# Performance work log

Measured on AMD Instinct MI355X. Metric: run time of the kernel, lower is better.

## Reference

```python
import jax, jax.numpy as jnp
import numpy as np

S, M, E, K, C = 4096, 512, 16, 2, 128
H1, H2, H3 = 500, 500, 2000
SAMPLE = int(np.percentile(np.arange(S), 90))  # = 3685, matches int(np.percentile(idx_set, 90))
KMUL, KNUM = 2.0, 5


def setup_inputs() -> dict:
    key = jax.random.key(0)
    ks = jax.random.split(key, 8)
    def init(k, shape, fan):
        return (jax.random.normal(k, shape, jnp.float32) / np.float32(np.sqrt(fan)))
    inp = {
        'x': jax.random.normal(ks[0], (S, M), jnp.float32),
        'noise': jax.random.uniform(ks[1], (S, E), jnp.float32),
        'Wr': jnp.zeros((E, M), jnp.float32),  # router weight is zeroed in reset_parameters
        'W1': init(ks[2], (E, H1, M), M), 'b1': jnp.zeros((E, H1), jnp.float32),
        'W2': init(ks[3], (E, H2, H1), H1), 'b2': jnp.zeros((E, H2), jnp.float32),
        'W3': init(ks[4], (E, H3, H2), H2), 'b3': jnp.zeros((E, H3), jnp.float32),
        'W4': init(ks[5], (E, C, H3), H3), 'b4': jnp.zeros((E, C), jnp.float32),
    }
    rng = np.random.RandomState(0)
    npairs = K * (K - 1) // 2
    inp['idx1'] = jnp.asarray(np.stack([rng.choice(S, SAMPLE, replace=False) for _ in range(npairs)]).astype(np.int32))
    inp['idx2'] = jnp.asarray(np.stack([rng.choice(S, SAMPLE, replace=False) for _ in range(npairs)]).astype(np.int32))
    return inp


def _mmd(source, target):
    # Gaussian-kernel MMD, same math as MMD_loss (fix_sigma=None path).
    ns = source.shape[0]
    n = ns + target.shape[0]
    total = jnp.concatenate([source, target], axis=0)            # [n, d]
    sq = jnp.sum(total * total, axis=-1)
    d2 = sq[:, None] + sq[None, :] - 2.0 * (total @ total.T)     # [n, n] squared L2
    bw = jax.lax.stop_gradient(d2).sum() / (n * n - n)           # .data in torch => stop_gradient
    bw = bw / (KMUL ** (KNUM // 2))
    kern = jnp.zeros_like(d2)
    for i in range(KNUM):
        kern = kern + jnp.exp(-d2 / (bw * (KMUL ** i)))
    xx = kern[:ns, :ns]
    yy = kern[ns:, ns:]
    xy = kern[:ns, ns:]
    yx = kern[ns:, :ns]
    return jnp.mean(xx + yy - xy - yx)


def _forward(x, noise, Wr, W1, b1, W2, b2, W3, b3, W4, b4, idx1, idx2):
    select = x @ Wr.T + noise                                    # [S, E]
    gate, index = jax.lax.top_k(select, K)                       # [S, K]
    mask = jax.nn.one_hot(index, E, dtype=select.dtype)          # [S, K, E]
    density = mask.mean(axis=-2)                                 # [S, E]
    density_proxy = select.mean(axis=-2)                         # [E]
    balance_loss = jnp.mean(density_proxy * density) * float(E ** 2)
    mask_flat = mask.sum(axis=-1)                                # [S, K] (all ones)
    combine = jnp.transpose(gate[..., None] * mask_flat[..., None] * mask, (0, 2, 1))  # [S, E, K]
    dispatch = (combine != 0).astype(combine.dtype)              # bool().to(dtype)
    select0 = dispatch
    expert_inputs = jnp.einsum('sm,sec->ecm', x, dispatch)       # [E, K, M]
    h = jax.nn.relu(jnp.einsum('ecm,ehm->ech', expert_inputs, W1) + b1[:, None, :])
    h = jax.nn.relu(jnp.einsum('ech,egh->ecg', h, W2) + b2[:, None, :])
    h = jax.nn.relu(jnp.einsum('ecg,efg->ecf', h, W3) + b3[:, None, :])
    eout = jnp.einsum('ecf,edf->ecd', h, W4) + b4[:, None, :]    # [E, K, C]
    middle = jnp.transpose(jnp.einsum('sec,ecm->scm', combine, eout), (1, 0, 2))  # [K, S, C]
    output = jnp.einsum('sec,ecm->sm', combine, eout)            # [S, C]
    dist_loss = jnp.float32(0.0)
    p = 0
    for i in range(K):
        for j in range(i + 1, K):
            dist_loss = dist_loss - _mmd(middle[i][idx1[p]], middle[j][idx2[p]])
            p += 1
    return output, select0, balance_loss, dist_loss


def reference(x, noise, Wr, W1, b1, W2, b2, W3, b3, W4, b4, idx1, idx2):
    return _forward(x, noise, Wr, W1, b1, W2, b2, W3, b3, W4, b4, idx1, idx2)
```

## Files before the change

kernel.cpp:

```cpp
#include <hip/hip_runtime.h>

constexpr int S = 4096, M = 512, E = 16, CC = 128;
constexpr int H1 = 500, H2 = 500, H3 = 2000;

__global__ void k_route(const float* __restrict__ x, const float* __restrict__ noise,
                        const float* __restrict__ Wr, int* __restrict__ i0, int* __restrict__ i1,
                        float* __restrict__ g0, float* __restrict__ g1,
                        float* __restrict__ sel0, float* __restrict__ selpart) {
  int wid = threadIdx.x >> 6, lane = threadIdx.x & 63;
  int s = blockIdx.x * 4 + wid;
  const float* xr = x + (size_t)s * M;
  float xv[8];
#pragma unroll
  for (int c = 0; c < 8; ++c) xv[c] = xr[lane + 64 * c];
  float v[E];
#pragma unroll
  for (int e = 0; e < E; ++e) {
    const float* wr = Wr + (size_t)e * M;
    float acc = 0.f;
#pragma unroll
    for (int c = 0; c < 8; ++c) acc = fmaf(xv[c], wr[lane + 64 * c], acc);
#pragma unroll
    for (int off = 32; off; off >>= 1) acc += __shfl_xor(acc, off);
    v[e] = acc + noise[s * E + e];
  }
  int a0 = 0; float m0 = v[0];
#pragma unroll
  for (int e = 1; e < E; ++e) if (v[e] > m0) { m0 = v[e]; a0 = e; }
  int a1 = -1; float m1 = -3.4e38f;
#pragma unroll
  for (int e = 0; e < E; ++e) if (e != a0 && v[e] > m1) { m1 = v[e]; a1 = e; }
  __shared__ float vsh[4][16];
  if (lane < 16) vsh[wid][lane] = v[lane];
  if (lane == 0) { i0[s] = a0; i1[s] = a1; g0[s] = m0; g1[s] = m1; }
  if (lane < 16) {
    int e = lane;
    sel0[(size_t)s * 32 + e * 2 + 0] = (e == a0 && m0 != 0.f) ? 1.f : 0.f;
    sel0[(size_t)s * 32 + e * 2 + 1] = (e == a1 && m1 != 0.f) ? 1.f : 0.f;
  }
  __syncthreads();
  if (threadIdx.x < 16) {
    int e = threadIdx.x;
    selpart[blockIdx.x * 16 + e] = vsh[0][e] + vsh[1][e] + vsh[2][e] + vsh[3][e];
  }
}

__global__ void k_balance(const float* __restrict__ selpart, const int* __restrict__ i0,
                          const int* __restrict__ i1, float* __restrict__ outb) {
  __shared__ double part[512];
  __shared__ float dpl[E];
  int t = threadIdx.x;
  int e = t & 15, r0 = t >> 4;
  double acc = 0.0;
  for (int b = r0; b < 1024; b += 32) acc += (double)selpart[b * 16 + e];
  part[t] = acc;
  __syncthreads();
  for (int off = 256; off >= 16; off >>= 1) {
    if (t < off) part[t] += part[t + off];
    __syncthreads();
  }
  if (t < E) dpl[t] = (float)(part[t] / (double)S);
  __syncthreads();
  double acc2 = 0.0;
  for (int s = t; s < S; s += 512) acc2 += 0.5 * ((double)dpl[i0[s]] + (double)dpl[i1[s]]);
  part[t] = acc2;
  __syncthreads();
  for (int off = 256; off; off >>= 1) {
    if (t < off) part[t] += part[t + off];
    __syncthreads();
  }
  if (t == 0) outb[0] = (float)(part[0] / 256.0);
}

__global__ void k_lists(const int* __restrict__ i0, const int* __restrict__ i1,
                        const float* __restrict__ g0, const float* __restrict__ g1,
                        int* __restrict__ list, int* __restrict__ cnt) {
  int ek = blockIdx.x;
  int k = ek & 1, e = ek >> 1;
  const int* route = k ? i1 : i0;
  const float* gg = k ? g1 : g0;
  __shared__ int base_s;
  __shared__ int wsum[4];
  int t = threadIdx.x;
  int lane = t & 63, w = t >> 6;
  if (t == 0) base_s = 0;
  __syncthreads();
  for (int s0 = 0; s0 < S; s0 += 256) {
    int s = s0 + t;
    bool flag = (route[s] == e) && (gg[s] != 0.f);
    unsigned long long m = __ballot(flag);
    int within = __popcll(m & ((1ull << lane) - 1ull));
    if (lane == 0) wsum[w] = __popcll(m);
    __syncthreads();
    int wbase = base_s;
    for (int i = 0; i < w; ++i) wbase += wsum[i];
    if (flag) list[ek * S + wbase + within] = s;
    __syncthreads();
    if (t == 0) base_s += wsum[0] + wsum[1] + wsum[2] + wsum[3];
    __syncthreads();
  }
  if (t == 0) cnt[ek] = base_s;
}

__global__ void k_gather(const float* __restrict__ x, const int* __restrict__ list,
                         const int* __restrict__ cnt, float* __restrict__ gpart) {
  int b = blockIdx.x;
  int seg = b & 7, chunk = (b >> 3) & 3, ek = b >> 5;
  int t = threadIdx.x;
  int d = chunk * 128 + t;
  int nl = cnt[ek];
  const int* lp = list + ek * S;
  float acc = 0.f;
  int q = seg;
  for (; q + 24 < nl; q += 32) {
    int s0 = lp[q], s1 = lp[q + 8], s2 = lp[q + 16], s3 = lp[q + 24];
    acc += x[(size_t)s0 * M + d];
    acc += x[(size_t)s1 * M + d];
    acc += x[(size_t)s2 * M + d];
    acc += x[(size_t)s3 * M + d];
  }
  for (; q < nl; q += 8) acc += x[(size_t)lp[q] * M + d];
  gpart[(size_t)seg * (32 * M) + ek * M + d] = acc;
}

__global__ void k_gather_red(const float* __restrict__ gpart, float* __restrict__ ei) {
  int idx = blockIdx.x * blockDim.x + threadIdx.x;
  float acc = 0.f;
#pragma unroll
  for (int sg = 0; sg < 8; ++sg) acc += gpart[(size_t)sg * (32 * M) + idx];
  ei[idx] = acc;
}

template <int DIN, int HOUT, bool RELU>
__global__ void k_layer(const float* __restrict__ in, const float* __restrict__ W,
                        const float* __restrict__ bias, float* __restrict__ out) {
  int w = (blockIdx.x * blockDim.x + threadIdx.x) >> 6;
  int lane = threadIdx.x & 63;
  if (w >= E * HOUT) return;
  int e = w / HOUT, h = w - e * HOUT;
  const float* wr = W + ((size_t)e * HOUT + h) * DIN;
  const float* in0 = in + (size_t)(e * 2 + 0) * DIN;
  const float* in1 = in + (size_t)(e * 2 + 1) * DIN;
  float a0 = 0.f, a1 = 0.f;
  for (int m = lane; m < DIN; m += 64) {
    float wv = wr[m];
    a0 += wv * in0[m];
    a1 += wv * in1[m];
  }
#pragma unroll
  for (int off = 32; off; off >>= 1) {
    a0 += __shfl_xor(a0, off);
    a1 += __shfl_xor(a1, off);
  }
  if (lane == 0) {
    float bb = bias[e * HOUT + h];
    float o0 = a0 + bb, o1 = a1 + bb;
    if (RELU) { o0 = fmaxf(o0, 0.f); o1 = fmaxf(o1, 0.f); }
    out[(size_t)(e * 2 + 0) * HOUT + h] = o0;
    out[(size_t)(e * 2 + 1) * HOUT + h] = o1;
  }
}

__global__ void k_output(const float* __restrict__ eo, const int* __restrict__ i0,
                         const int* __restrict__ i1, const float* __restrict__ g0,
                         const float* __restrict__ g1, float* __restrict__ out) {
  int idx = blockIdx.x * blockDim.x + threadIdx.x;
  if (idx >= S * CC) return;
  int s = idx >> 7, d = idx & (CC - 1);
  out[idx] = g0[s] * eo[(i0[s] * 2 + 0) * CC + d] + g1[s] * eo[(i1[s] * 2 + 1) * CC + d];
}

__global__ void k_G(const float* __restrict__ eo, float* __restrict__ G32) {
  __shared__ float Es[32][129];
  int t = threadIdx.x;
  for (int i = t; i < 32 * 128; i += 256) Es[i >> 7][i & 127] = eo[i];
  __syncthreads();
  for (int p = t; p < 1024; p += 256) {
    int u = p >> 5, v = p & 31;
    float s = 0.f;
#pragma unroll 8
    for (int d = 0; d < 128; ++d) s = fmaf(Es[u][d], Es[v][d], s);
    G32[p] = s;
  }
}

__global__ void k_rows(const int* __restrict__ idx1, const int* __restrict__ idx2,
                       const int* __restrict__ i0, const int* __restrict__ i1,
                       const float* __restrict__ g0, const float* __restrict__ g1,
                       const float* __restrict__ G32, float* __restrict__ rowg,
                       float* __restrict__ rowa, int* __restrict__ rowe,
                       int ns, int ncnt, int npad) {
  int r = blockIdx.x * 256 + threadIdx.x;
  if (r >= npad) return;
  float g = 0.f; int ek = 0;
  if (r < ns)        { int t = idx1[r];      ek = i0[t] * 2 + 0; g = g0[t]; }
  else if (r < ncnt) { int t = idx2[r - ns]; ek = i1[t] * 2 + 1; g = g1[t]; }
  rowg[r] = g;
  rowe[r] = ek;
  rowa[r] = g * g * G32[ek * 32 + ek];
}

__global__ void k_prep(const float* __restrict__ rowg, const float* __restrict__ rowa,
                       const int* __restrict__ rowe, const float* __restrict__ G32,
                       float* __restrict__ cl, int ncnt) {
  __shared__ float ws[256 * 33];
  __shared__ double red[256];
  __shared__ float wfin[32];
  int t = threadIdx.x;
#pragma unroll
  for (int e = 0; e < 32; ++e) ws[t * 33 + e] = 0.f;
  double asum = 0.0;
  for (int r = t; r < ncnt; r += 256) {
    asum += (double)rowa[r];
    ws[t * 33 + rowe[r]] += rowg[r];
  }
  red[t] = asum;
  __syncthreads();
  if (t < 32) {
    float sw = 0.f;
    for (int q = 0; q < 256; ++q) sw += ws[q * 33 + t];
    wfin[t] = sw;
  }
  for (int off = 128; off; off >>= 1) { if (t < off) red[t] += red[t + off]; __syncthreads(); }
  double asum_tot = red[0];
  __syncthreads();
  double part = 0.0;
  for (int i = t; i < 1024; i += 256)
    part += (double)wfin[i >> 5] * (double)wfin[i & 31] * (double)G32[i];
  red[t] = part;
  __syncthreads();
  for (int off = 128; off; off >>= 1) { if (t < off) red[t] += red[t + off]; __syncthreads(); }
  if (t == 0) {
    double nn = (double)ncnt;
    double sumd2 = 2.0 * nn * asum_tot - 2.0 * red[0];
    double bw = sumd2 / (nn * nn - nn) / 4.0;
#pragma unroll
    for (int l = 0; l < 5; ++l) cl[l] = (float)(1.0 / (bw * (double)(1 << l)));
  }
}

__global__ __launch_bounds__(256) void k_mmd(const float* __restrict__ rowg,
                      const float* __restrict__ rowa, const int* __restrict__ rowe,
                      const float* __restrict__ G32, const float* __restrict__ cl,
                      double* __restrict__ bsum, int ns, int ncnt, int nt) {
  int L = blockIdx.x;
  int bi = 0, rem = L;
  while (rem >= nt - bi) { rem -= nt - bi; ++bi; }
  int bj = bi + rem;
  const int ib = bi * 128, jb = bj * 128;

  __shared__ float K2[32 * 33];
  __shared__ float gAs[136], aAs[136], gBs[136], aBs[136];
  __shared__ int eAs[136], eBs[136];
  __shared__ float rsum[256];
  int tid = threadIdx.x;
  float c = cl[4];
  for (int i = tid; i < 1024; i += 256) K2[(i >> 5) * 33 + (i & 31)] = 2.f * c * G32[i];
  if (tid < 128) {
    int p = (tid & 7) * 17 + (tid >> 3);
    gAs[p] = rowg[ib + tid]; aAs[p] = c * rowa[ib + tid]; eAs[p] = rowe[ib + tid] * 33;
    gBs[p] = rowg[jb + tid]; aBs[p] = c * rowa[jb + tid]; eBs[p] = rowe[jb + tid];
  }
  __syncthreads();

  int ti = tid & 15, tj = tid >> 4;
  float gi[8], Ai[8], sgi[8], gj[8], Aj[8], sgj[8];
  int ei[8], ej[8];
#pragma unroll
  for (int r = 0; r < 8; ++r) {
    int i = ti * 8 + r, p = r * 17 + ti;
    gi[r] = gAs[p]; Ai[r] = aAs[p]; ei[r] = eAs[p];
    int m = ib + i;
    sgi[r] = (m < ns) ? 1.f : (m < ncnt ? -1.f : 0.f);
    int j = tj * 8 + r, q = r * 17 + tj;
    gj[r] = gBs[q]; Aj[r] = aBs[q]; ej[r] = eBs[q];
    int nn2 = jb + j;
    sgj[r] = (nn2 < ns) ? 1.f : (nn2 < ncnt ? -1.f : 0.f);
  }

  float tsum = 0.f;
#pragma unroll
  for (int r = 0; r < 8; ++r) {
#pragma unroll
    for (int q = 0; q < 8; ++q) {
      float gg = gi[r] * gj[q];
      float arg = fmaf(K2[ei[r] + ej[q]], gg, -(Ai[r] + Aj[q]));
      float t = __expf(arg);
      float t2 = t * t;   float s5 = t + t2;
      float t4 = t2 * t2; s5 += t4;
      float t8 = t4 * t4; s5 += t8;
      float t16 = t8 * t8; s5 += t16;
      tsum = fmaf(sgi[r] * sgj[q], s5, tsum);
    }
  }
  rsum[tid] = tsum;
  __syncthreads();
  for (int off = 128; off; off >>= 1) {
    if (tid < off) rsum[tid] += rsum[tid + off];
    __syncthreads();
  }
  if (tid == 0) bsum[L] = (double)rsum[0] * ((bi == bj) ? 1.0 : 2.0);
}

__global__ void k_final(const double* __restrict__ bsum, int nb, int ns, float* __restrict__ outp) {
  __shared__ double red[256];
  int t = threadIdx.x;
  double acc = 0.0;
  for (int i = t; i < nb; i += 256) acc += bsum[i];
  red[t] = acc;
  __syncthreads();
  for (int off = 128; off; off >>= 1) { if (t < off) red[t] += red[t + off]; __syncthreads(); }
  if (t == 0) outp[0] = (float)(-red[0] / ((double)ns * (double)ns));
}

extern "C" void kernel_launch(void* const* d_in, const int* in_sizes, int n_in,
                              void* d_out, int out_size, void* d_ws, size_t ws_size,
                              hipStream_t stream) {
  const float* x  = (const float*)d_in[0];
  const float* noise = (const float*)d_in[1];
  const float* Wr = (const float*)d_in[2];
  const float* W1 = (const float*)d_in[3];
  const float* b1 = (const float*)d_in[4];
  const float* W2 = (const float*)d_in[5];
  const float* b2 = (const float*)d_in[6];
  const float* W3 = (const float*)d_in[7];
  const float* b3 = (const float*)d_in[8];
  const float* W4 = (const float*)d_in[9];
  const float* b4 = (const float*)d_in[10];
  const int* idx1 = (const int*)d_in[11];
  const int* idx2 = (const int*)d_in[12];
  int ns = in_sizes[11];
  int n = 2 * ns;
  int npad = (n + 127) & ~127;
  int nt = npad / 128;
  int ntri = nt * (nt + 1) / 2;

  char* wp = (char*)d_ws;
  size_t off = 0;
  auto alloc = [&](size_t bytes) -> void* {
    void* p = wp + off;
    off += (bytes + 255) & ~(size_t)255;
    return p;
  };
  int*   i0  = (int*)alloc((size_t)S * 4);
  int*   i1  = (int*)alloc((size_t)S * 4);
  float* g0  = (float*)alloc((size_t)S * 4);
  float* g1  = (float*)alloc((size_t)S * 4);
  float* selpart = (float*)alloc((size_t)1024 * 16 * 4);
  int*   list = (int*)alloc((size_t)32 * S * 4);
  int*   cnt  = (int*)alloc(32 * 4);
  float* gpart = (float*)alloc((size_t)8 * 32 * M * 4);
  float* ei  = (float*)alloc((size_t)E * 2 * M * 4);
  float* h1  = (float*)alloc((size_t)E * 2 * H1 * 4);
  float* h2  = (float*)alloc((size_t)E * 2 * H2 * 4);
  float* h3  = (float*)alloc((size_t)E * 2 * H3 * 4);
  float* eo  = (float*)alloc((size_t)E * 2 * CC * 4);
  float* G32 = (float*)alloc((size_t)1024 * 4);
  float* rowg = (float*)alloc((size_t)npad * 4);
  float* rowa = (float*)alloc((size_t)npad * 4);
  int*   rowe = (int*)alloc((size_t)npad * 4);
  float* cl  = (float*)alloc(8 * 4);
  double* bsum = (double*)alloc((size_t)ntri * 8);
  (void)ws_size; (void)n_in; (void)out_size;

  float* out      = (float*)d_out;
  float* out_sel0 = out + (size_t)S * CC;
  float* out_bal  = out + (size_t)S * CC + (size_t)S * E * 2;
  float* out_dist = out_bal + 1;

  k_route<<<S / 4, 256, 0, stream>>>(x, noise, Wr, i0, i1, g0, g1, out_sel0, selpart);
  k_balance<<<1, 512, 0, stream>>>(selpart, i0, i1, out_bal);
  k_lists<<<32, 256, 0, stream>>>(i0, i1, g0, g1, list, cnt);
  k_gather<<<1024, 128, 0, stream>>>(x, list, cnt, gpart);
  k_gather_red<<<64, 256, 0, stream>>>(gpart, ei);
  k_layer<M, H1, true><<<(E * H1 + 3) / 4, 256, 0, stream>>>(ei, W1, b1, h1);
  k_layer<H1, H2, true><<<(E * H2 + 3) / 4, 256, 0, stream>>>(h1, W2, b2, h2);
  k_layer<H2, H3, true><<<(E * H3 + 3) / 4, 256, 0, stream>>>(h2, W3, b3, h3);
  k_layer<H3, CC, false><<<(E * CC + 3) / 4, 256, 0, stream>>>(h3, W4, b4, eo);
  k_output<<<(S * CC) / 256, 256, 0, stream>>>(eo, i0, i1, g0, g1, out);
  k_G<<<1, 256, 0, stream>>>(eo, G32);
  k_rows<<<(npad + 255) / 256, 256, 0, stream>>>(idx1, idx2, i0, i1, g0, g1, G32,
                                                 rowg, rowa, rowe, ns, n, npad);
  k_prep<<<1, 256, 0, stream>>>(rowg, rowa, rowe, G32, cl, n);
  k_mmd<<<ntri, 256, 0, stream>>>(rowg, rowa, rowe, G32, cl, bsum, ns, n, nt);
  k_final<<<1, 256, 0, stream>>>(bsum, ntri, ns, out_dist);
}
```

Measured before the change: 132.0 us.

## Fuse MoE tail kernels via last-block atomic counters and merge gather passes

Cuts the launch sequence from about fifteen kernels to seven. The list build, gather and gather reduction become a single kernel that scans routes held in shared memory. Balance loss, G-matrix, row prep and bandwidth computation move into the last-finishing block of the layer-4 kernel, and the output combine, MMD tiles and final reduction share one launch that also uses a last-block counter. The aim is to remove launch overhead and serial single-block kernels, at the cost of a full 4096-row scan per gather block and serial tail work inside one block.

```diff
diff --git a/kernel.cpp b/kernel.cpp
--- a/kernel.cpp
+++ b/kernel.cpp
@@ -6,7 +6,9 @@
 __global__ void k_route(const float* __restrict__ x, const float* __restrict__ noise,
                         const float* __restrict__ Wr, int* __restrict__ i0, int* __restrict__ i1,
                         float* __restrict__ g0, float* __restrict__ g1,
-                        float* __restrict__ sel0, float* __restrict__ selpart) {
+                        float* __restrict__ sel0, float* __restrict__ selpart,
+                        int* __restrict__ counters) {
+  if (blockIdx.x == 0 && threadIdx.x == 0) { counters[0] = 0; counters[1] = 0; }
   int wid = threadIdx.x >> 6, lane = threadIdx.x & 63;
   int s = blockIdx.x * 4 + wid;
   const float* xr = x + (size_t)s * M;
@@ -45,90 +47,36 @@
   }
 }
 
-__global__ void k_balance(const float* __restrict__ selpart, const int* __restrict__ i0,
-                          const int* __restrict__ i1, float* __restrict__ outb) {
-  __shared__ double part[512];
-  __shared__ float dpl[E];
-  int t = threadIdx.x;
-  int e = t & 15, r0 = t >> 4;
-  double acc = 0.0;
-  for (int b = r0; b < 1024; b += 32) acc += (double)selpart[b * 16 + e];
-  part[t] = acc;
-  __syncthreads();
-  for (int off = 256; off >= 16; off >>= 1) {
-    if (t < off) part[t] += part[t + off];
-    __syncthreads();
-  }
-  if (t < E) dpl[t] = (float)(part[t] / (double)S);
-  __syncthreads();
-  double acc2 = 0.0;
-  for (int s = t; s < S; s += 512) acc2 += 0.5 * ((double)dpl[i0[s]] + (double)dpl[i1[s]]);
-  part[t] = acc2;
-  __syncthreads();
-  for (int off = 256; off; off >>= 1) {
-    if (t < off) part[t] += part[t + off];
-    __syncthreads();
-  }
-  if (t == 0) outb[0] = (float)(part[0] / 256.0);
-}
-
-__global__ void k_lists(const int* __restrict__ i0, const int* __restrict__ i1,
+__global__ __launch_bounds__(1024) void k_gather(const float* __restrict__ x,
+                        const int* __restrict__ i0, const int* __restrict__ i1,
                         const float* __restrict__ g0, const float* __restrict__ g1,
-                        int* __restrict__ list, int* __restrict__ cnt) {
-  int ek = blockIdx.x;
+                        float* __restrict__ ei) {
+  __shared__ int rsi[S];
+  __shared__ float rsg[S];
+  __shared__ float gacc[8][128];
+  int b = blockIdx.x;
+  int chunk = b & 3, ek = b >> 2;
   int k = ek & 1, e = ek >> 1;
   const int* route = k ? i1 : i0;
   const float* gg = k ? g1 : g0;
-  __shared__ int base_s;
-  __shared__ int wsum[4];
   int t = threadIdx.x;
-  int lane = t & 63, w = t >> 6;
-  if (t == 0) base_s = 0;
-  __syncthreads();
-  for (int s0 = 0; s0 < S; s0 += 256) {
-    int s = s0 + t;
-    bool flag = (route[s] == e) && (gg[s] != 0.f);
-    unsigned long long m = __ballot(flag);
-    int within = __popcll(m & ((1ull << lane) - 1ull));
-    if (lane == 0) wsum[w] = __popcll(m);
-    __syncthreads();
-    int wbase = base_s;
-    for (int i = 0; i < w; ++i) wbase += wsum[i];
-    if (flag) list[ek * S + wbase + within] = s;
-    __syncthreads();
-    if (t == 0) base_s += wsum[0] + wsum[1] + wsum[2] + wsum[3];
-    __syncthreads();
-  }
-  if (t == 0) cnt[ek] = base_s;
-}
-
-__global__ void k_gather(const float* __restrict__ x, const int* __restrict__ list,
-                         const int* __restrict__ cnt, float* __restrict__ gpart) {
-  int b = blockIdx.x;
-  int seg = b & 7, chunk = (b >> 3) & 3, ek = b >> 5;
-  int t = threadIdx.x;
-  int d = chunk * 128 + t;
-  int nl = cnt[ek];
-  const int* lp = list + ek * S;
+  for (int i = t; i < S; i += 1024) { rsi[i] = route[i]; rsg[i] = gg[i]; }
+  __syncthreads();
+  int g = t >> 7, dl = t & 127;
+  int d = chunk * 128 + dl;
   float acc = 0.f;
-  int q = seg;
-  for (; q + 24 < nl; q += 32) {
-    int s0 = lp[q], s1 = lp[q + 8], s2 = lp[q + 16], s3 = lp[q + 24];
-    acc += x[(size_t)s0 * M + d];
-    acc += x[(size_t)s1 * M + d];
-    acc += x[(size_t)s2 * M + d];
-    acc += x[(size_t)s3 * M + d];
-  }
-  for (; q < nl; q += 8) acc += x[(size_t)lp[q] * M + d];
-  gpart[(size_t)seg * (32 * M) + ek * M + d] = acc;
-}
-
-__global__ void k_gather_red(const float* __restrict__ gpart, float* __restrict__ ei) {
-  int idx = blockIdx.x * blockDim.x + threadIdx.x;
-  float acc = 0.f;
-#pragma unroll
-  for (int sg = 0; sg < 8; ++sg) acc += gpart[(size_t)sg * (32 * M) + idx];
-  ei[idx] = acc;
+  int q0 = g * 512;
+  for (int q = q0; q < q0 + 512; ++q) {
+    if (rsi[q] == e && rsg[q] != 0.f) acc += x[(size_t)q * M + d];
+  }
+  gacc[g][dl] = acc;
+  __syncthreads();
+  if (t < 128) {
+    float ssum = 0.f;
+#pragma unroll
+    for (int g2 = 0; g2 < 8; ++g2) ssum += gacc[g2][t];
+    ei[ek * M + chunk * 128 + t] = ssum;
+  }
 }
 
 template <int DIN, int HOUT, bool RELU>
@@ -161,99 +109,153 @@
   }
 }
 
-__global__ void k_output(const float* __restrict__ eo, const int* __restrict__ i0,
-                         const int* __restrict__ i1, const float* __restrict__ g0,
-                         const float* __restrict__ g1, float* __restrict__ out) {
-  int idx = blockIdx.x * blockDim.x + threadIdx.x;
-  if (idx >= S * CC) return;
-  int s = idx >> 7, d = idx & (CC - 1);
-  out[idx] = g0[s] * eo[(i0[s] * 2 + 0) * CC + d] + g1[s] * eo[(i1[s] * 2 + 1) * CC + d];
-}
-
-__global__ void k_G(const float* __restrict__ eo, float* __restrict__ G32) {
-  __shared__ float Es[32][129];
+__global__ __launch_bounds__(256) void k_l4(const float* __restrict__ h3in,
+                        const float* __restrict__ W4, const float* __restrict__ b4,
+                        float* __restrict__ eo,
+                        const int* __restrict__ idx1, const int* __restrict__ idx2,
+                        const int* __restrict__ i0, const int* __restrict__ i1,
+                        const float* __restrict__ g0, const float* __restrict__ g1,
+                        const float* __restrict__ selpart,
+                        float* __restrict__ G32, float* __restrict__ rowg,
+                        float* __restrict__ rowa, int* __restrict__ rowe,
+                        float* __restrict__ cl, float* __restrict__ outb,
+                        int ns, int ncnt, int npad, int* __restrict__ counters) {
+  int w = (blockIdx.x * 256 + threadIdx.x) >> 6;
+  int lane = threadIdx.x & 63;
+  {
+    int e = w / CC, h = w - e * CC;
+    const float* wr = W4 + ((size_t)e * CC + h) * H3;
+    const float* in0 = h3in + (size_t)(e * 2 + 0) * H3;
+    const float* in1 = h3in + (size_t)(e * 2 + 1) * H3;
+    float a0 = 0.f, a1 = 0.f;
+    for (int m = lane; m < H3; m += 64) {
+      float wv = wr[m];
+      a0 += wv * in0[m];
+      a1 += wv * in1[m];
+    }
+#pragma unroll
+    for (int off = 32; off; off >>= 1) {
+      a0 += __shfl_xor(a0, off);
+      a1 += __shfl_xor(a1, off);
+    }
+    if (lane == 0) {
+      float bb = b4[e * CC + h];
+      eo[(size_t)(e * 2 + 0) * CC + h] = a0 + bb;
+      eo[(size_t)(e * 2 + 1) * CC + h] = a1 + bb;
+    }
+  }
+  __shared__ int lastflag;
+  __syncthreads();
+  if (threadIdx.x == 0) {
+    __threadfence();
+    int old = atomicAdd(&counters[0], 1);
+    lastflag = (old == (int)gridDim.x - 1) ? 1 : 0;
+  }
+  __syncthreads();
+  if (!lastflag) return;
+  __threadfence();
+
+  __shared__ float u_s[256 * 33];
+  __shared__ float Gs[1024];
+  __shared__ double red_d[256];
+  __shared__ float wf[32];
+  __shared__ float dpl[16];
   int t = threadIdx.x;
-  for (int i = t; i < 32 * 128; i += 256) Es[i >> 7][i & 127] = eo[i];
+
+  for (int i = t; i < 32 * 128; i += 256) u_s[(i >> 7) * 132 + (i & 127)] = eo[i];
   __syncthreads();
   for (int p = t; p < 1024; p += 256) {
     int u = p >> 5, v = p & 31;
     float s = 0.f;
 #pragma unroll 8
-    for (int d = 0; d < 128; ++d) s = fmaf(Es[u][d], Es[v][d], s);
-    G32[p] = s;
-  }
-}
-
-__global__ void k_rows(const int* __restrict__ idx1, const int* __restrict__ idx2,
-                       const int* __restrict__ i0, const int* __restrict__ i1,
-                       const float* __restrict__ g0, const float* __restrict__ g1,
-                       const float* __restrict__ G32, float* __restrict__ rowg,
-                       float* __restrict__ rowa, int* __restrict__ rowe,
-                       int ns, int ncnt, int npad) {
-  int r = blockIdx.x * 256 + threadIdx.x;
-  if (r >= npad) return;
-  float g = 0.f; int ek = 0;
-  if (r < ns)        { int t = idx1[r];      ek = i0[t] * 2 + 0; g = g0[t]; }
-  else if (r < ncnt) { int t = idx2[r - ns]; ek = i1[t] * 2 + 1; g = g1[t]; }
-  rowg[r] = g;
-  rowe[r] = ek;
-  rowa[r] = g * g * G32[ek * 32 + ek];
-}
-
-__global__ void k_prep(const float* __restrict__ rowg, const float* __restrict__ rowa,
-                       const int* __restrict__ rowe, const float* __restrict__ G32,
-                       float* __restrict__ cl, int ncnt) {
-  __shared__ float ws[256 * 33];
-  __shared__ double red[256];
-  __shared__ float wfin[32];
-  int t = threadIdx.x;
-#pragma unroll
-  for (int e = 0; e < 32; ++e) ws[t * 33 + e] = 0.f;
+    for (int d2 = 0; d2 < 128; ++d2) s = fmaf(u_s[u * 132 + d2], u_s[v * 132 + d2], s);
+    Gs[p] = s; G32[p] = s;
+  }
+  __syncthreads();
+
+  for (int e2 = 0; e2 < 33; ++e2) u_s[t * 33 + e2] = 0.f;
   double asum = 0.0;
-  for (int r = t; r < ncnt; r += 256) {
-    asum += (double)rowa[r];
-    ws[t * 33 + rowe[r]] += rowg[r];
-  }
-  red[t] = asum;
+  for (int r = t; r < npad; r += 256) {
+    float g = 0.f; int ek = 0;
+    if (r < ns)        { int tk = idx1[r];      ek = i0[tk] * 2 + 0; g = g0[tk]; }
+    else if (r < ncnt) { int tk = idx2[r - ns]; ek = i1[tk] * 2 + 1; g = g1[tk]; }
+    rowg[r] = g; rowe[r] = ek;
+    float a = g * g * Gs[ek * 32 + ek];
+    rowa[r] = a;
+    asum += (double)a;
+    u_s[t * 33 + ek] += g;
+  }
+  red_d[t] = asum;
   __syncthreads();
   if (t < 32) {
     float sw = 0.f;
-    for (int q = 0; q < 256; ++q) sw += ws[q * 33 + t];
-    wfin[t] = sw;
-  }
-  for (int off = 128; off; off >>= 1) { if (t < off) red[t] += red[t + off]; __syncthreads(); }
-  double asum_tot = red[0];
+    for (int q = 0; q < 256; ++q) sw += u_s[q * 33 + t];
+    wf[t] = sw;
+  }
+  for (int off = 128; off; off >>= 1) { if (t < off) red_d[t] += red_d[t + off]; __syncthreads(); }
+  double asum_tot = red_d[0];
   __syncthreads();
   double part = 0.0;
   for (int i = t; i < 1024; i += 256)
-    part += (double)wfin[i >> 5] * (double)wfin[i & 31] * (double)G32[i];
-  red[t] = part;
-  __syncthreads();
-  for (int off = 128; off; off >>= 1) { if (t < off) red[t] += red[t + off]; __syncthreads(); }
+    part += (double)wf[i >> 5] * (double)wf[i & 31] * (double)Gs[i];
+  red_d[t] = part;
+  __syncthreads();
+  for (int off = 128; off; off >>= 1) { if (t < off) red_d[t] += red_d[t + off]; __syncthreads(); }
   if (t == 0) {
     double nn = (double)ncnt;
-    double sumd2 = 2.0 * nn * asum_tot - 2.0 * red[0];
+    double sumd2 = 2.0 * nn * asum_tot - 2.0 * red_d[0];
     double bw = sumd2 / (nn * nn - nn) / 4.0;
 #pragma unroll
     for (int l = 0; l < 5; ++l) cl[l] = (float)(1.0 / (bw * (double)(1 << l)));
   }
-}
-
-__global__ __launch_bounds__(256) void k_mmd(const float* __restrict__ rowg,
-                      const float* __restrict__ rowa, const int* __restrict__ rowe,
-                      const float* __restrict__ G32, const float* __restrict__ cl,
-                      double* __restrict__ bsum, int ns, int ncnt, int nt) {
-  int L = blockIdx.x;
+  __syncthreads();
+
+  {
+    int e2 = t & 15, r0 = t >> 4;
+    double acc = 0.0;
+    for (int b2 = r0; b2 < 1024; b2 += 16) acc += (double)selpart[b2 * 16 + e2];
+    red_d[t] = acc;
+    __syncthreads();
+    for (int off = 128; off >= 16; off >>= 1) { if (t < off) red_d[t] += red_d[t + off]; __syncthreads(); }
+    if (t < 16) dpl[t] = (float)(red_d[t] / (double)S);
+    __syncthreads();
+    double acc2 = 0.0;
+    for (int s2 = t; s2 < S; s2 += 256) acc2 += 0.5 * ((double)dpl[i0[s2]] + (double)dpl[i1[s2]]);
+    red_d[t] = acc2;
+    __syncthreads();
+    for (int off = 128; off; off >>= 1) { if (t < off) red_d[t] += red_d[t + off]; __syncthreads(); }
+    if (t == 0) outb[0] = (float)(red_d[0] / 256.0);
+  }
+}
+
+__global__ __launch_bounds__(256) void k_tail(const float* __restrict__ eo,
+                      const int* __restrict__ i0, const int* __restrict__ i1,
+                      const float* __restrict__ g0, const float* __restrict__ g1,
+                      float* __restrict__ out,
+                      const float* __restrict__ rowg, const float* __restrict__ rowa,
+                      const int* __restrict__ rowe, const float* __restrict__ G32,
+                      const float* __restrict__ cl, double* __restrict__ bsum,
+                      float* __restrict__ out_dist,
+                      int ns, int ncnt, int nt, int ntri, int* __restrict__ counters) {
+  __shared__ float K2[32 * 33];
+  __shared__ float gAs[136], aAs[136], gBs[136], aBs[136];
+  __shared__ int eAs[136], eBs[136];
+  __shared__ float rsum[256];
+  __shared__ double redf[256];
+  __shared__ int lastflag;
+  int b = blockIdx.x, tid = threadIdx.x;
+  if (b < 2048) {
+    int idx = b * 256 + tid;
+    int s = idx >> 7, d = idx & (CC - 1);
+    out[idx] = g0[s] * eo[(i0[s] * 2 + 0) * CC + d] + g1[s] * eo[(i1[s] * 2 + 1) * CC + d];
+    return;
+  }
+  int L = b - 2048;
   int bi = 0, rem = L;
   while (rem >= nt - bi) { rem -= nt - bi; ++bi; }
   int bj = bi + rem;
   const int ib = bi * 128, jb = bj * 128;
 
-  __shared__ float K2[32 * 33];
-  __shared__ float gAs[136], aAs[136], gBs[136], aBs[136];
-  __shared__ int eAs[136], eBs[136];
-  __shared__ float rsum[256];
-  int tid = threadIdx.x;
   float c = cl[4];
   for (int i = tid; i < 1024; i += 256) K2[(i >> 5) * 33 + (i & 31)] = 2.f * c * G32[i];
   if (tid < 128) {
@@ -300,17 +302,21 @@
     __syncthreads();
   }
   if (tid == 0) bsum[L] = (double)rsum[0] * ((bi == bj) ? 1.0 : 2.0);
-}
-
-__global__ void k_final(const double* __restrict__ bsum, int nb, int ns, float* __restrict__ outp) {
-  __shared__ double red[256];
-  int t = threadIdx.x;
+
+  if (tid == 0) {
+    __threadfence();
+    int old = atomicAdd(&counters[1], 1);
+    lastflag = (old == ntri - 1) ? 1 : 0;
+  }
+  __syncthreads();
+  if (!lastflag) return;
+  __threadfence();
   double acc = 0.0;
-  for (int i = t; i < nb; i += 256) acc += bsum[i];
-  red[t] = acc;
-  __syncthreads();
-  for (int off = 128; off; off >>= 1) { if (t < off) red[t] += red[t + off]; __syncthreads(); }
-  if (t == 0) outp[0] = (float)(-red[0] / ((double)ns * (double)ns));
+  for (int i = tid; i < ntri; i += 256) acc += bsum[i];
+  redf[tid] = acc;
+  __syncthreads();
+  for (int off = 128; off; off >>= 1) { if (tid < off) redf[tid] += redf[tid + off]; __syncthreads(); }
+  if (tid == 0) out_dist[0] = (float)(-redf[0] / ((double)ns * (double)ns));
 }
 
 extern "C" void kernel_launch(void* const* d_in, const int* in_sizes, int n_in,
@@ -347,9 +353,6 @@
   float* g0  = (float*)alloc((size_t)S * 4);
   float* g1  = (float*)alloc((size_t)S * 4);
   float* selpart = (float*)alloc((size_t)1024 * 16 * 4);
-  int*   list = (int*)alloc((size_t)32 * S * 4);
-  int*   cnt  = (int*)alloc(32 * 4);
-  float* gpart = (float*)alloc((size_t)8 * 32 * M * 4);
   float* ei  = (float*)alloc((size_t)E * 2 * M * 4);
   float* h1  = (float*)alloc((size_t)E * 2 * H1 * 4);
   float* h2  = (float*)alloc((size_t)E * 2 * H2 * 4);
@@ -361,6 +364,7 @@
   int*   rowe = (int*)alloc((size_t)npad * 4);
   float* cl  = (float*)alloc(8 * 4);
   double* bsum = (double*)alloc((size_t)ntri * 8);
+  int* counters = (int*)alloc(256);
   (void)ws_size; (void)n_in; (void)out_size;
 
   float* out      = (float*)d_out;
@@ -368,20 +372,14 @@
   float* out_bal  = out + (size_t)S * CC + (size_t)S * E * 2;
   float* out_dist = out_bal + 1;
 
-  k_route<<<S / 4, 256, 0, stream>>>(x, noise, Wr, i0, i1, g0, g1, out_sel0, selpart);
-  k_balance<<<1, 512, 0, stream>>>(selpart, i0, i1, out_bal);
-  k_lists<<<32, 256, 0, stream>>>(i0, i1, g0, g1, list, cnt);
-  k_gather<<<1024, 128, 0, stream>>>(x, list, cnt, gpart);
-  k_gather_red<<<64, 256, 0, stream>>>(gpart, ei);
+  k_route<<<S / 4, 256, 0, stream>>>(x, noise, Wr, i0, i1, g0, g1, out_sel0, selpart, counters);
+  k_gather<<<128, 1024, 0, stream>>>(x, i0, i1, g0, g1, ei);
   k_layer<M, H1, true><<<(E * H1 + 3) / 4, 256, 0, stream>>>(ei, W1, b1, h1);
   k_layer<H1, H2, true><<<(E * H2 + 3) / 4, 256, 0, stream>>>(h1, W2, b2, h2);
   k_layer<H2, H3, true><<<(E * H3 + 3) / 4, 256, 0, stream>>>(h2, W3, b3, h3);
-  k_layer<H3, CC, false><<<(E * CC + 3) / 4, 256, 0, stream>>>(h3, W4, b4, eo);
-  k_output<<<(S * CC) / 256, 256, 0, stream>>>(eo, i0, i1, g0, g1, out);
-  k_G<<<1, 256, 0, stream>>>(eo, G32);
-  k_rows<<<(npad + 255) / 256, 256, 0, stream>>>(idx1, idx2, i0, i1, g0, g1, G32,
-                                                 rowg, rowa, rowe, ns, n, npad);
-  k_prep<<<1, 256, 0, stream>>>(rowg, rowa, rowe, G32, cl, n);
-  k_mmd<<<ntri, 256, 0, stream>>>(rowg, rowa, rowe, G32, cl, bsum, ns, n, nt);
-  k_final<<<1, 256, 0, stream>>>(bsum, ntri, ns, out_dist);
-}
+  k_l4<<<(E * CC) / 4, 256, 0, stream>>>(h3, W4, b4, eo, idx1, idx2, i0, i1, g0, g1,
+                                         selpart, G32, rowg, rowa, rowe, cl, out_bal,
+                                         ns, n, npad, counters);
+  k_tail<<<2048 + ntri, 256, 0, stream>>>(eo, i0, i1, g0, g1, out, rowg, rowa, rowe,
+                                          G32, cl, bsum, out_dist, ns, n, nt, ntri, counters);
+}
```

New measurement: 190.8 us. +44.6%, slower.

## Fuse output scatter and final reduction into enlarged MMD kernel

Applied to the files above, without the earlier changes.

Merges the k_output gather/combine and the k_final reduction into the MMD kernel. Extra blocks compute the output rows, and the last finishing MMD block, found with an atomic counter, does the final sum. MMD tiles grow from 128 to 256 rows per side with 512-thread blocks, and the block reduction now uses wave shuffles. This removes two kernel launches and the tail reduction launch. In exchange it adds a threadfence/atomic handshake, more registers per thread, and fewer, larger tiles that could lower occupancy.

```diff
diff --git a/kernel.cpp b/kernel.cpp
--- a/kernel.cpp
+++ b/kernel.cpp
@@ -2,11 +2,14 @@
 
 constexpr int S = 4096, M = 512, E = 16, CC = 128;
 constexpr int H1 = 500, H2 = 500, H3 = 2000;
+constexpr int TB = 256;
 
 __global__ void k_route(const float* __restrict__ x, const float* __restrict__ noise,
                         const float* __restrict__ Wr, int* __restrict__ i0, int* __restrict__ i1,
                         float* __restrict__ g0, float* __restrict__ g1,
-                        float* __restrict__ sel0, float* __restrict__ selpart) {
+                        float* __restrict__ sel0, float* __restrict__ selpart,
+                        int* __restrict__ counters) {
+  if (blockIdx.x == 0 && threadIdx.x == 0) { counters[0] = 0; }
   int wid = threadIdx.x >> 6, lane = threadIdx.x & 63;
   int s = blockIdx.x * 4 + wid;
   const float* xr = x + (size_t)s * M;
@@ -161,15 +164,6 @@
   }
 }
 
-__global__ void k_output(const float* __restrict__ eo, const int* __restrict__ i0,
-                         const int* __restrict__ i1, const float* __restrict__ g0,
-                         const float* __restrict__ g1, float* __restrict__ out) {
-  int idx = blockIdx.x * blockDim.x + threadIdx.x;
-  if (idx >= S * CC) return;
-  int s = idx >> 7, d = idx & (CC - 1);
-  out[idx] = g0[s] * eo[(i0[s] * 2 + 0) * CC + d] + g1[s] * eo[(i1[s] * 2 + 1) * CC + d];
-}
-
 __global__ void k_G(const float* __restrict__ eo, float* __restrict__ G32) {
   __shared__ float Es[32][129];
   int t = threadIdx.x;
@@ -239,78 +233,105 @@
   }
 }
 
-__global__ __launch_bounds__(256) void k_mmd(const float* __restrict__ rowg,
+__global__ __launch_bounds__(512) void k_mmd2(const float* __restrict__ rowg,
                       const float* __restrict__ rowa, const int* __restrict__ rowe,
                       const float* __restrict__ G32, const float* __restrict__ cl,
-                      double* __restrict__ bsum, int ns, int ncnt, int nt) {
-  int L = blockIdx.x;
-  int bi = 0, rem = L;
+                      const float* __restrict__ eo,
+                      const int* __restrict__ i0, const int* __restrict__ i1,
+                      const float* __restrict__ g0, const float* __restrict__ g1,
+                      float* __restrict__ out, double* __restrict__ bsum,
+                      float* __restrict__ out_dist,
+                      int ns, int ncnt, int nt, int ntri, int* __restrict__ counters) {
+  int b = blockIdx.x, tid = threadIdx.x;
+  if (b >= ntri) {
+    int idx = (b - ntri) * 512 + tid;
+    int s = idx >> 7, d = idx & (CC - 1);
+    out[idx] = g0[s] * eo[(i0[s] * 2 + 0) * CC + d] + g1[s] * eo[(i1[s] * 2 + 1) * CC + d];
+    return;
+  }
+  __shared__ float K2[1056];
+  __shared__ float gA[264], aA[264], sA[264];
+  __shared__ int   eA[264];
+  __shared__ float gB[264], aB[264], sB[264];
+  __shared__ int   eB[264];
+  __shared__ float wred[8];
+  __shared__ double redd[512];
+  __shared__ int lastflag;
+
+  int bi = 0, rem = b;
   while (rem >= nt - bi) { rem -= nt - bi; ++bi; }
   int bj = bi + rem;
-  const int ib = bi * 128, jb = bj * 128;
-
-  __shared__ float K2[32 * 33];
-  __shared__ float gAs[136], aAs[136], gBs[136], aBs[136];
-  __shared__ int eAs[136], eBs[136];
-  __shared__ float rsum[256];
-  int tid = threadIdx.x;
+  const int ib = bi * TB, jb = bj * TB;
+
   float c = cl[4];
-  for (int i = tid; i < 1024; i += 256) K2[(i >> 5) * 33 + (i & 31)] = 2.f * c * G32[i];
-  if (tid < 128) {
-    int p = (tid & 7) * 17 + (tid >> 3);
-    gAs[p] = rowg[ib + tid]; aAs[p] = c * rowa[ib + tid]; eAs[p] = rowe[ib + tid] * 33;
-    gBs[p] = rowg[jb + tid]; aBs[p] = c * rowa[jb + tid]; eBs[p] = rowe[jb + tid];
+  for (int i = tid; i < 1024; i += 512) K2[(i >> 5) * 33 + (i & 31)] = 2.f * c * G32[i];
+  if (tid < TB) {
+    int r = tid, p = (r & 7) * 33 + (r >> 3);
+    int m = ib + r;
+    gA[p] = rowg[m]; aA[p] = c * rowa[m]; eA[p] = rowe[m] * 33;
+    sA[p] = (m < ns) ? 1.f : (m < ncnt ? -1.f : 0.f);
+  } else {
+    int r = tid - TB, p = (r & 7) * 33 + (r >> 3);
+    int m = jb + r;
+    gB[p] = rowg[m]; aB[p] = c * rowa[m]; eB[p] = rowe[m];
+    sB[p] = (m < ns) ? 1.f : (m < ncnt ? -1.f : 0.f);
   }
   __syncthreads();
 
   int ti = tid & 15, tj = tid >> 4;
-  float gi[8], Ai[8], sgi[8], gj[8], Aj[8], sgj[8];
-  int ei[8], ej[8];
-#pragma unroll
-  for (int r = 0; r < 8; ++r) {
-    int i = ti * 8 + r, p = r * 17 + ti;
-    gi[r] = gAs[p]; Ai[r] = aAs[p]; ei[r] = eAs[p];
-    int m = ib + i;
-    sgi[r] = (m < ns) ? 1.f : (m < ncnt ? -1.f : 0.f);
-    int j = tj * 8 + r, q = r * 17 + tj;
-    gj[r] = gBs[q]; Aj[r] = aBs[q]; ej[r] = eBs[q];
-    int nn2 = jb + j;
-    sgj[r] = (nn2 < ns) ? 1.f : (nn2 < ncnt ? -1.f : 0.f);
+  float gj[8], Aj[8], sgj[8]; int exj[8];
+#pragma unroll
+  for (int q = 0; q < 8; ++q) {
+    int p = q * 33 + tj;
+    gj[q] = gB[p]; Aj[q] = aB[p]; exj[q] = eB[p]; sgj[q] = sB[p];
+  }
+  float gi[16], Ai[16], sgi[16]; int exi[16];
+#pragma unroll
+  for (int r = 0; r < 16; ++r) {
+    int p = (r & 7) * 33 + ti * 2 + (r >> 3);
+    gi[r] = gA[p]; Ai[r] = aA[p]; exi[r] = eA[p]; sgi[r] = sA[p];
   }
 
   float tsum = 0.f;
 #pragma unroll
-  for (int r = 0; r < 8; ++r) {
+  for (int r = 0; r < 16; ++r) {
 #pragma unroll
     for (int q = 0; q < 8; ++q) {
       float gg = gi[r] * gj[q];
-      float arg = fmaf(K2[ei[r] + ej[q]], gg, -(Ai[r] + Aj[q]));
-      float t = __expf(arg);
-      float t2 = t * t;   float s5 = t + t2;
-      float t4 = t2 * t2; s5 += t4;
-      float t8 = t4 * t4; s5 += t8;
-      float t16 = t8 * t8; s5 += t16;
+      float arg = fmaf(K2[exi[r] + exj[q]], gg, -(Ai[r] + Aj[q]));
+      float tv = __expf(arg);
+      float t2 = tv * tv;   float s5 = tv + t2;
+      float t4 = t2 * t2;   s5 += t4;
+      float t8 = t4 * t4;   s5 += t8;
+      float t16 = t8 * t8;  s5 += t16;
       tsum = fmaf(sgi[r] * sgj[q], s5, tsum);
     }
   }
-  rsum[tid] = tsum;
-  __syncthreads();
-  for (int off = 128; off; off >>= 1) {
-    if (tid < off) rsum[tid] += rsum[tid + off];
-    __syncthreads();
-  }
-  if (tid == 0) bsum[L] = (double)rsum[0] * ((bi == bj) ? 1.0 : 2.0);
-}
-
-__global__ void k_final(const double* __restrict__ bsum, int nb, int ns, float* __restrict__ outp) {
-  __shared__ double red[256];
-  int t = threadIdx.x;
+#pragma unroll
+  for (int off = 32; off; off >>= 1) tsum += __shfl_xor(tsum, off);
+  if ((tid & 63) == 0) wred[tid >> 6] = tsum;
+  __syncthreads();
+  if (tid == 0) {
+    float sblk = 0.f;
+#pragma unroll
+    for (int w = 0; w < 8; ++w) sblk += wred[w];
+    bsum[b] = (double)sblk * ((bi == bj) ? 1.0 : 2.0);
+  }
+
+  if (tid == 0) {
+    __threadfence();
+    int old = atomicAdd(&counters[0], 1);
+    lastflag = (old == ntri - 1) ? 1 : 0;
+  }
+  __syncthreads();
+  if (!lastflag) return;
+  __threadfence();
   double acc = 0.0;
-  for (int i = t; i < nb; i += 256) acc += bsum[i];
-  red[t] = acc;
-  __syncthreads();
-  for (int off = 128; off; off >>= 1) { if (t < off) red[t] += red[t + off]; __syncthreads(); }
-  if (t == 0) outp[0] = (float)(-red[0] / ((double)ns * (double)ns));
+  for (int i = tid; i < ntri; i += 512) acc += bsum[i];
+  redd[tid] = acc;
+  __syncthreads();
+  for (int off = 256; off; off >>= 1) { if (tid < off) redd[tid] += redd[tid + off]; __syncthreads(); }
+  if (tid == 0) out_dist[0] = (float)(-redd[0] / ((double)ns * (double)ns));
 }
 
 extern "C" void kernel_launch(void* const* d_in, const int* in_sizes, int n_in,
@@ -331,8 +352,8 @@
   const int* idx2 = (const int*)d_in[12];
   int ns = in_sizes[11];
   int n = 2 * ns;
-  int npad = (n + 127) & ~127;
-  int nt = npad / 128;
+  int npad = (n + 255) & ~255;
+  int nt = npad / TB;
   int ntri = nt * (nt + 1) / 2;
 
   char* wp = (char*)d_ws;
@@ -361,6 +382,7 @@
   int*   rowe = (int*)alloc((size_t)npad * 4);
   float* cl  = (float*)alloc(8 * 4);
   double* bsum = (double*)alloc((size_t)ntri * 8);
+  int* counters = (int*)alloc(256);
   (void)ws_size; (void)n_in; (void)out_size;
 
   float* out      = (float*)d_out;
@@ -368,7 +390,7 @@
   float* out_bal  = out + (size_t)S * CC + (size_t)S * E * 2;
   float* out_dist = out_bal + 1;
 
-  k_route<<<S / 4, 256, 0, stream>>>(x, noise, Wr, i0, i1, g0, g1, out_sel0, selpart);
+  k_route<<<S / 4, 256, 0, stream>>>(x, noise, Wr, i0, i1, g0, g1, out_sel0, selpart, counters);
   k_balance<<<1, 512, 0, stream>>>(selpart, i0, i1, out_bal);
   k_lists<<<32, 256, 0, stream>>>(i0, i1, g0, g1, list, cnt);
   k_gather<<<1024, 128, 0, stream>>>(x, list, cnt, gpart);
@@ -377,11 +399,11 @@
   k_layer<H1, H2, true><<<(E * H2 + 3) / 4, 256, 0, stream>>>(h1, W2, b2, h2);
   k_layer<H2, H3, true><<<(E * H3 + 3) / 4, 256, 0, stream>>>(h2, W3, b3, h3);
   k_layer<H3, CC, false><<<(E * CC + 3) / 4, 256, 0, stream>>>(h3, W4, b4, eo);
-  k_output<<<(S * CC) / 256, 256, 0, stream>>>(eo, i0, i1, g0, g1, out);
   k_G<<<1, 256, 0, stream>>>(eo, G32);
   k_rows<<<(npad + 255) / 256, 256, 0, stream>>>(idx1, idx2, i0, i1, g0, g1, G32,
                                                  rowg, rowa, rowe, ns, n, npad);
   k_prep<<<1, 256, 0, stream>>>(rowg, rowa, rowe, G32, cl, n);
-  k_mmd<<<ntri, 256, 0, stream>>>(rowg, rowa, rowe, G32, cl, bsum, ns, n, nt);
-  k_final<<<1, 256, 0, stream>>>(bsum, ntri, ns, out_dist);
-}
+  k_mmd2<<<ntri + (S * CC) / 512, 512, 0, stream>>>(rowg, rowa, rowe, G32, cl, eo,
+                                                    i0, i1, g0, g1, out, bsum, out_dist,
+                                                    ns, n, nt, ntri, counters);
+}
```

Result: slower. 135.4 us (+2.6%).
